# Performance work log

Hardware: AMD Instinct MI355X
Metric: run time of the kernel (lower is better)

Reference implementation:

```python
import jax, jax.numpy as jnp
import numpy as np

DEPTH = 3
MAX_NB = 10
HIDDEN = 128


def setup_inputs() -> dict:
    key = jax.random.key(0)
    k = jax.random.split(key, 14)
    B, A, E, H, NB = 64, 1024, 2048, HIDDEN, MAX_NB
    s = 0.05
    return {
        "input_atom": jax.random.normal(k[0], (B, A, 82), jnp.float32),
        "input_bond": jax.random.normal(k[1], (B, E, 6), jnp.float32),
        "atom_graph": jax.random.randint(k[2], (B, A, NB), 0, A),
        "bond_graph": jax.random.randint(k[3], (B, A, NB), 0, E),
        "num_nbs": jax.random.randint(k[4], (B, A), 0, NB + 1),
        "node_mask": jnp.ones((B, A), jnp.float32),
        "W_atom": jax.random.normal(k[5], (82, H), jnp.float32) * s,
        "W_nei_atom": jax.random.normal(k[6], (H, H), jnp.float32) * s,
        "W_nei_bond": jax.random.normal(k[7], (6, H), jnp.float32) * s,
        "W_self": jax.random.normal(k[8], (H, H), jnp.float32) * s,
        "W_U2": jax.random.normal(k[9], (H + 6, H), jnp.float32) * s,
        "b_U2": jax.random.normal(k[10], (H,), jnp.float32) * s,
        "W_U1": jax.random.normal(k[11], (2 * H, H), jnp.float32) * s,
        "b_U1": jax.random.normal(k[12], (H,), jnp.float32) * s,
    }


def reference(input_atom, input_bond, atom_graph, bond_graph, num_nbs, node_mask,
              W_atom, W_nei_atom, W_nei_bond, W_self, W_U2, b_U2, W_U1, b_U1):
    B, A, NB = atom_graph.shape
    H = W_atom.shape[1]
    atom_features = input_atom @ W_atom                       # [B, A, H]
    # neighbor validity mask: [B, A, NB, 1]
    mask_nei = (jnp.arange(NB)[None, None, :] < num_nbs[:, :, None]).astype(jnp.float32)[..., None]
    idx_a = atom_graph.reshape(B, A * NB, 1)
    idx_b = bond_graph.reshape(B, A * NB, 1)
    # bond neighbor features are loop-invariant: gather once
    fbond_nei = jnp.take_along_axis(input_bond, idx_b, axis=1).reshape(B, A, NB, 6)
    h_nei_bond = fbond_nei @ W_nei_bond                       # [B, A, NB, H]
    node_m = node_mask[..., None]                             # [B, A, 1]
    kernel = None
    for _ in range(DEPTH):
        fatom_nei = jnp.take_along_axis(atom_features, idx_a, axis=1).reshape(B, A, NB, H)
        h_nei = (fatom_nei @ W_nei_atom) * h_nei_bond         # [B, A, NB, H]
        f_nei = jnp.sum(h_nei * mask_nei, axis=2)             # [B, A, H]
        f_self = atom_features @ W_self                        # [B, A, H]
        kernel = f_nei * f_self * node_m
        l_nei = jnp.concatenate([fatom_nei, fbond_nei], axis=3)  # [B, A, NB, H+6]
        pre_label = l_nei @ W_U2 + b_U2
        nei_label = jnp.sum(pre_label * mask_nei, axis=2)      # [B, A, H]
        new_label = jnp.concatenate([atom_features, nei_label], axis=2)
        atom_features = new_label @ W_U1 + b_U1
    return kernel, atom_features
```

## Files before the change

### kernel.cpp

```cpp
#include <hip/hip_runtime.h>

constexpr int NB = 10, H = 128;
constexpr int M = 64 * 1024;
constexpr long SL = (long)M * H;

typedef __attribute__((ext_vector_type(8))) short s16x8;
typedef __attribute__((ext_vector_type(4))) float f32x4;

__device__ __forceinline__ ushort f2b(float f) {
    union { float f; uint u; } v; v.f = f;
    uint u = v.u;
    uint r = u + 0x7fffu + ((u >> 16) & 1u);
    return (ushort)(r >> 16);
}
__device__ __forceinline__ float b2f(ushort u) {
    union { uint u; float f; } v; v.u = ((uint)u) << 16; return v.f;
}

__device__ __forceinline__ int swz(int bid, int cpx) {
    return (bid & 7) * cpx + (bid >> 3);
}

template<int NC, int FLAGS>
__device__ __forceinline__ void gemm_body(
    int tg, const ushort* __restrict__ Abf, const ushort* __restrict__ WT,
    const ushort* __restrict__ FNb, const float* __restrict__ nmask,
    float* __restrict__ Cf, ushort* __restrict__ Cb)
{
    constexpr bool KOUT = FLAGS & 8, OF32 = FLAGS & 16;
    constexpr int K = NC * 32;
    const int lane = threadIdx.x & 63, wid = threadIdx.x >> 6;
    const int l15 = lane & 15, g = lane >> 4;

    s16x8 w[2][NC];
    #pragma unroll
    for (int ct = 0; ct < 2; ++ct)
        #pragma unroll
        for (int kc = 0; kc < NC; ++kc)
            w[ct][kc] = *(const s16x8*)(WT + (size_t)((2 * wid + ct) * 16 + l15) * K + kc * 32 + g * 8);

    #pragma unroll
    for (int i = 0; i < 4; ++i) {
        const int m0 = (tg * 4 + i) * 16;
        s16x8 ac[NC];
        #pragma unroll
        for (int kc = 0; kc < NC; ++kc)
            ac[kc] = *(const s16x8*)(Abf + (size_t)(m0 + l15) * K + kc * 32 + g * 8);

        f32x4 acc[2];
        #pragma unroll
        for (int ct = 0; ct < 2; ++ct) acc[ct] = (f32x4){0.f, 0.f, 0.f, 0.f};
        #pragma unroll
        for (int kc = 0; kc < NC; ++kc)
            #pragma unroll
            for (int ct = 0; ct < 2; ++ct)
                acc[ct] = __builtin_amdgcn_mfma_f32_16x16x32_bf16(ac[kc], w[ct][kc], acc[ct], 0, 0, 0);

        #pragma unroll
        for (int ct = 0; ct < 2; ++ct) {
            const int col = (2 * wid + ct) * 16 + l15;
            #pragma unroll
            for (int r = 0; r < 4; ++r) {
                const int m = m0 + 4 * g + r;
                const size_t o = (size_t)m * H + col;
                float v = acc[ct][r];
                if constexpr (KOUT) v = v * b2f(FNb[o]) * nmask[m];
                if constexpr (OF32) Cf[o] = v; else Cb[o] = f2b(v);
            }
        }
    }
}

template<bool OF32>
__device__ __forceinline__ void u1f_body(
    int tg, const ushort* __restrict__ AF, const ushort* __restrict__ SATOM,
    const ushort* __restrict__ FBSb, const ushort* __restrict__ WT,
    float* __restrict__ Cf, ushort* __restrict__ Cb)
{
    const int lane = threadIdx.x & 63, wid = threadIdx.x >> 6;
    const int l15 = lane & 15, g = lane >> 4;

    s16x8 w[2][9];
    #pragma unroll
    for (int ct = 0; ct < 2; ++ct)
        #pragma unroll
        for (int kc = 0; kc < 9; ++kc)
            w[ct][kc] = *(const s16x8*)(WT + (size_t)((2 * wid + ct) * 16 + l15) * 288 + kc * 32 + g * 8);
    #pragma unroll
    for (int ct = 0; ct < 2; ++ct)
        #pragma unroll
        for (int kc = 0; kc < 9; ++kc)
            asm volatile("" : "+v"(w[ct][kc]));

    #pragma unroll
    for (int i = 0; i < 4; ++i) {
        const int m0 = (tg * 4 + i) * 16;
        const size_t rb = (size_t)(m0 + l15) * H + g * 8;
        s16x8 ac[9];
        #pragma unroll
        for (int kc = 0; kc < 4; ++kc) {
            ac[kc]     = *(const s16x8*)(AF    + rb + kc * 32);
            ac[kc + 4] = *(const s16x8*)(SATOM + rb + kc * 32);
        }
        ac[8] = (s16x8){0,0,0,0,0,0,0,0};
        if (g == 0) ac[8] = *(const s16x8*)(FBSb + (size_t)(m0 + l15) * 8);

        f32x4 acc[2];
        #pragma unroll
        for (int ct = 0; ct < 2; ++ct) acc[ct] = (f32x4){0.f, 0.f, 0.f, 0.f};
        #pragma unroll
        for (int kc = 0; kc < 9; ++kc)
            #pragma unroll
            for (int ct = 0; ct < 2; ++ct)
                acc[ct] = __builtin_amdgcn_mfma_f32_16x16x32_bf16(ac[kc], w[ct][kc], acc[ct], 0, 0, 0);

        #pragma unroll
        for (int ct = 0; ct < 2; ++ct) {
            const int col = (2 * wid + ct) * 16 + l15;
            #pragma unroll
            for (int r = 0; r < 4; ++r) {
                const size_t o = (size_t)(m0 + 4 * g + r) * H + col;
                if constexpr (OF32) Cf[o] = acc[ct][r]; else Cb[o] = f2b(acc[ct][r]);
            }
        }
    }
}

template<int NC, int FLAGS>
__global__ __launch_bounds__(256, 4) void gemm_af(
    const ushort* __restrict__ Abf, const ushort* __restrict__ WT,
    const ushort* __restrict__ FNb, const float* __restrict__ nmask,
    float* __restrict__ Cf, ushort* __restrict__ Cb)
{
    gemm_body<NC, FLAGS>(swz(blockIdx.x, 128), Abf, WT, FNb, nmask, Cf, Cb);
}

template<bool OF32>
__global__ __launch_bounds__(256, 3) void u1f(
    const ushort* __restrict__ AF, const ushort* __restrict__ SATOM,
    const ushort* __restrict__ FBSb, const ushort* __restrict__ WT,
    float* __restrict__ Cf, ushort* __restrict__ Cb)
{
    u1f_body<OF32>(swz(blockIdx.x, 128), AF, SATOM, FBSb, WT, Cf, Cb);
}

__global__ __launch_bounds__(256, 3) void final2(
    const ushort* __restrict__ AF, const ushort* __restrict__ SATl,
    const ushort* __restrict__ FBSb, const ushort* __restrict__ WTu1f,
    const ushort* __restrict__ WTslf, const ushort* __restrict__ FNEIb,
    const float* __restrict__ nmask, float* __restrict__ out1,
    float* __restrict__ out0)
{
    if (blockIdx.x < 1024)
        u1f_body<true>(swz(blockIdx.x, 128), AF, SATl, FBSb, WTu1f, out1, nullptr);
    else
        gemm_body<4, 8 | 16>(swz(blockIdx.x - 1024, 128), AF, WTslf, FNEIb,
                             nmask, out0, nullptr);
}

__global__ __launch_bounds__(256, 8) void gather_satom(
    const ushort* __restrict__ AF, const int* __restrict__ ag,
    const int* __restrict__ nn, ushort* __restrict__ SATOM)
{
    const int bid = swz(blockIdx.x, 512);
    const int m  = bid * 16 + (threadIdx.x >> 4);
    const int c8 = (threadIdx.x & 15) * 8;
    const int b  = m >> 10;
    const int nnb = nn[m];
    const ushort* AFb = AF + ((size_t)b << 10) * H + c8;
    const int* agm = ag + (size_t)m * NB;

    int2 iv0 = *(const int2*)(agm + 0);
    int2 iv1 = *(const int2*)(agm + 2);
    int2 iv2 = *(const int2*)(agm + 4);
    int2 iv3 = *(const int2*)(agm + 6);
    int2 iv4 = *(const int2*)(agm + 8);

    float sacc[8];
    #pragma unroll
    for (int i = 0; i < 8; ++i) sacc[i] = 0.f;

    #define GS_STEP(nb, ia)                                              \
    if ((nb) < nnb) {                                                    \
        s16x8 av = *(const s16x8*)(AFb + (size_t)(ia) * H);              \
        _Pragma("unroll")                                                \
        for (int i = 0; i < 8; ++i) sacc[i] += b2f((ushort)av[i]);       \
    }
    GS_STEP(0, iv0.x) GS_STEP(1, iv0.y)
    GS_STEP(2, iv1.x) GS_STEP(3, iv1.y)
    GS_STEP(4, iv2.x) GS_STEP(5, iv2.y)
    GS_STEP(6, iv3.x) GS_STEP(7, iv3.y)
    GS_STEP(8, iv4.x) GS_STEP(9, iv4.y)
    #undef GS_STEP

    s16x8 so;
    #pragma unroll
    for (int i = 0; i < 8; ++i) so[i] = (short)f2b(sacc[i]);
    *(s16x8*)(SATOM + (size_t)m * H + c8) = so;
}

__global__ __launch_bounds__(256, 4) void gather_last(
    const ushort* __restrict__ AF, const ushort* __restrict__ ATW,
    const ushort* __restrict__ HB, const int* __restrict__ ag,
    const int* __restrict__ bg, const int* __restrict__ nn,
    ushort* __restrict__ SATOM, ushort* __restrict__ FNEIb)
{
    const int bid = swz(blockIdx.x, 512);
    const int m  = bid * 16 + (threadIdx.x >> 4);
    const int c8 = (threadIdx.x & 15) * 8;
    const int b  = m >> 10;
    const int nnb = nn[m];
    const ushort* AFb  = AF  + ((size_t)b << 10) * H + c8;
    const ushort* ATWb = ATW + ((size_t)b << 10) * H + c8;
    const ushort* HBb  = HB  + ((size_t)b << 11) * H + c8;
    const int* agm = ag + (size_t)m * NB;
    const int* bgm = bg + (size_t)m * NB;

    int2 ia0 = *(const int2*)(agm + 0), ib0 = *(const int2*)(bgm + 0);
    int2 ia1 = *(const int2*)(agm + 2), ib1 = *(const int2*)(bgm + 2);
    int2 ia2 = *(const int2*)(agm + 4), ib2 = *(const int2*)(bgm + 4);
    int2 ia3 = *(const int2*)(agm + 6), ib3 = *(const int2*)(bgm + 6);
    int2 ia4 = *(const int2*)(agm + 8), ib4 = *(const int2*)(bgm + 8);

    float sacc[8], facc[8];
    #pragma unroll
    for (int i = 0; i < 8; ++i) { sacc[i] = 0.f; facc[i] = 0.f; }

    #define GL_STEP(nb, ia, ib)                                          \
    if ((nb) < nnb) {                                                    \
        s16x8 av = *(const s16x8*)(AFb  + (size_t)(ia) * H);             \
        s16x8 tv = *(const s16x8*)(ATWb + (size_t)(ia) * H);             \
        s16x8 hv = *(const s16x8*)(HBb  + (size_t)(ib) * H);             \
        _Pragma("unroll")                                                \
        for (int i = 0; i < 8; ++i) {                                    \
            sacc[i] += b2f((ushort)av[i]);                               \
            facc[i] += b2f((ushort)tv[i]) * b2f((ushort)hv[i]);          \
        }                                                                \
    }
    GL_STEP(0, ia0.x, ib0.x) GL_STEP(1, ia0.y, ib0.y)
    GL_STEP(2, ia1.x, ib1.x) GL_STEP(3, ia1.y, ib1.y)
    GL_STEP(4, ia2.x, ib2.x) GL_STEP(5, ia2.y, ib2.y)
    GL_STEP(6, ia3.x, ib3.x) GL_STEP(7, ia3.y, ib3.y)
    GL_STEP(8, ia4.x, ib4.x) GL_STEP(9, ia4.y, ib4.y)
    #undef GL_STEP

    s16x8 so, fo;
    #pragma unroll
    for (int i = 0; i < 8; ++i) { so[i] = (short)f2b(sacc[i]); fo[i] = (short)f2b(facc[i]); }
    *(s16x8*)(SATOM + (size_t)m * H + c8) = so;
    *(s16x8*)(FNEIb + (size_t)m * H + c8) = fo;
}

__device__ __forceinline__ void fa_body(
    int tg, const float* __restrict__ ia, const float* __restrict__ Wa,
    ushort* __restrict__ Cb)
{
    const int lane = threadIdx.x & 63, wid = threadIdx.x >> 6;
    const int l15 = lane & 15, g = lane >> 4;

    s16x8 w[2][3];
    #pragma unroll
    for (int ct = 0; ct < 2; ++ct) {
        const int n = (2 * wid + ct) * 16 + l15;
        #pragma unroll
        for (int kc = 0; kc < 3; ++kc) {
            s16x8 wv;
            #pragma unroll
            for (int i = 0; i < 8; ++i) {
                const int k = kc * 32 + g * 8 + i;
                wv[i] = (short)(k < 82 ? f2b(Wa[k * H + n]) : 0);
            }
            w[ct][kc] = wv;
        }
    }

    #pragma unroll
    for (int t = 0; t < 4; ++t) {
        const int m0 = (tg * 4 + t) * 16;
        const float* row = ia + (size_t)(m0 + l15) * 82;
        s16x8 a[3];
        #pragma unroll
        for (int kc = 0; kc < 3; ++kc) {
            #pragma unroll
            for (int p = 0; p < 4; ++p) {
                const int k = kc * 32 + g * 8 + 2 * p;
                float2 v = (k < 82) ? *(const float2*)(row + k)
                                    : make_float2(0.f, 0.f);
                a[kc][2 * p]     = (short)f2b(v.x);
                a[kc][2 * p + 1] = (short)f2b(v.y);
            }
        }
        f32x4 acc[2];
        #pragma unroll
        for (int ct = 0; ct < 2; ++ct) acc[ct] = (f32x4){0.f, 0.f, 0.f, 0.f};
        #pragma unroll
        for (int kc = 0; kc < 3; ++kc)
            #pragma unroll
            for (int ct = 0; ct < 2; ++ct)
                acc[ct] = __builtin_amdgcn_mfma_f32_16x16x32_bf16(a[kc], w[ct][kc], acc[ct], 0, 0, 0);
        #pragma unroll
        for (int ct = 0; ct < 2; ++ct) {
            const int col = (2 * wid + ct) * 16 + l15;
            #pragma unroll
            for (int r = 0; r < 4; ++r)
                Cb[(size_t)(m0 + 4 * g + r) * H + col] = f2b(acc[ct][r]);
        }
    }
}

__global__ __launch_bounds__(256, 4) void k0_prep_fa(
    const float* __restrict__ ia, const float* __restrict__ Wa,
    const float* __restrict__ Wna, const float* __restrict__ Ws,
    const float* __restrict__ Wu2, const float* __restrict__ bu2,
    const float* __restrict__ Wu1, const float* __restrict__ bu1,
    const float* __restrict__ bond, const int* __restrict__ bg,
    const int* __restrict__ nn, const float* __restrict__ Wnb,
    ushort* __restrict__ AF0, ushort* __restrict__ WTs,
    ushort* __restrict__ FBSb, ushort* __restrict__ HB)
{
    const int bid = blockIdx.x;
    if (bid < 1024) {
        fa_body(swz(bid, 128), ia, Wa, AF0);
    } else if (bid < 1296) {
        int t = (bid - 1024) * 256 + threadIdx.x;
        const int tid = t;
        if (t < 128 * 128) { int n = t / 128, k = t % 128;
            WTs[tid] = f2b(Wna[k * H + n]); return; }
        t -= 128 * 128;
        if (t < 128 * 128) { int n = t / 128, k = t % 128;
            WTs[tid] = f2b(Ws[k * H + n]); return; }
        t -= 128 * 128;
        {
            const int n = t / 288, k = t % 288;
            float v = 0.f;
            if (k < 128) {
                v = Wu1[k * H + n];
            } else if (k < 256) {
                const int kk = k - 128;
                float s = 0.f;
                for (int j = 0; j < 128; ++j) s += Wu2[kk * H + j] * Wu1[(128 + j) * H + n];
                v = s;
            } else {
                const int j = k - 256;
                if (j < 6) {
                    float s = 0.f;
                    for (int q = 0; q < 128; ++q) s += Wu2[(128 + j) * H + q] * Wu1[(128 + q) * H + n];
                    v = s;
                } else if (j == 6) {
                    float s = 0.f;
                    for (int q = 0; q < 128; ++q) s += bu2[q] * Wu1[(128 + q) * H + n];
                    v = s;
                } else if (j == 7) {
                    v = bu1[n];
                }
            }
            WTs[tid] = f2b(v);
            return;
        }
    } else if (bid < 1552) {
        const int m = (bid - 1296) * 256 + threadIdx.x;
        const int b = m >> 10;
        const int nnb = nn[m];
        float s[6] = {0,0,0,0,0,0};
        for (int nb = 0; nb < nnb; ++nb) {
            const int ib = bg[m * NB + nb];
            const float* fb = bond + ((size_t)(b << 11) + (size_t)ib) * 6;
            #pragma unroll
            for (int j = 0; j < 6; ++j) s[j] += fb[j];
        }
        s16x8 o;
        #pragma unroll
        for (int j = 0; j < 6; ++j) o[j] = (short)f2b(s[j]);
        o[6] = (short)f2b((float)nnb);
        o[7] = (short)f2b(1.0f);
        *(s16x8*)(FBSb + (size_t)m * 8) = o;
    } else {
        const int t = (bid - 1552) * 256 + threadIdx.x;
        const int r = t >> 4, c8 = (t & 15) * 8;
        const float* fb = bond + (size_t)r * 6;
        const float2 f01 = *(const float2*)fb;
        const float2 f23 = *(const float2*)(fb + 2);
        const float2 f45 = *(const float2*)(fb + 4);
        s16x8 o;
        #pragma unroll
        for (int i = 0; i < 8; ++i) {
            const int c = c8 + i;
            const float v = f01.x * Wnb[0 * H + c] + f01.y * Wnb[1 * H + c]
                          + f23.x * Wnb[2 * H + c] + f23.y * Wnb[3 * H + c]
                          + f45.x * Wnb[4 * H + c] + f45.y * Wnb[5 * H + c];
            o[i] = (short)f2b(v);
        }
        *(s16x8*)(HB + (size_t)r * H + c8) = o;
    }
}

extern "C" void kernel_launch(void* const* d_in, const int* in_sizes, int n_in,
                              void* d_out, int out_size, void* d_ws, size_t ws_size,
                              hipStream_t stream)
{
    (void)in_sizes; (void)n_in; (void)out_size; (void)ws_size;

    const float* input_atom = (const float*)d_in[0];
    const float* input_bond = (const float*)d_in[1];
    const int*   atom_graph = (const int*)d_in[2];
    const int*   bond_graph = (const int*)d_in[3];
    const int*   num_nbs    = (const int*)d_in[4];
    const float* node_mask  = (const float*)d_in[5];
    const float* W_atom     = (const float*)d_in[6];
    const float* W_nei_atom = (const float*)d_in[7];
    const float* W_nei_bond = (const float*)d_in[8];
    const float* W_self     = (const float*)d_in[9];
    const float* W_U2       = (const float*)d_in[10];
    const float* b_U2       = (const float*)d_in[11];
    const float* W_U1       = (const float*)d_in[12];
    const float* b_U1       = (const float*)d_in[13];

    char* ws = (char*)d_ws;
    const size_t MB = 1024 * 1024;
    ushort* AF0   = (ushort*)(ws);
    ushort* AF1   = (ushort*)(ws + 16 * MB);
    ushort* SATw  = (ushort*)(ws + 32 * MB);
    ushort* ATW   = SATw;
    ushort* HB    = (ushort*)(ws + 64 * MB);
    ushort* SATl  = (ushort*)(ws + 96 * MB);
    ushort* FBSb  = (ushort*)(ws + 112 * MB);
    ushort* WTs_  = (ushort*)(ws + 113 * MB);

    ushort* WTna  = WTs_;
    ushort* WTslf = WTna  + 128 * 128;
    ushort* WTu1f = WTslf + 128 * 128;

    float*  out0  = (float*)d_out;
    float*  out1  = out0 + SL;
    ushort* FNEIb = AF1;

    k0_prep_fa<<<9744, 256, 0, stream>>>(input_atom, W_atom, W_nei_atom,
                                         W_self, W_U2, b_U2, W_U1, b_U1,
                                         input_bond, bond_graph, num_nbs,
                                         W_nei_bond, AF0, WTs_, FBSb, HB);

    gather_satom<<<4096, 256, 0, stream>>>(AF0, atom_graph, num_nbs, SATw);
    u1f<false><<<1024, 256, 0, stream>>>(AF0, SATw, FBSb, WTu1f, nullptr, AF1);
    gather_satom<<<4096, 256, 0, stream>>>(AF1, atom_graph, num_nbs, SATw);
    u1f<false><<<1024, 256, 0, stream>>>(AF1, SATw, FBSb, WTu1f, nullptr, AF0);

    gemm_af<4, 0><<<1024, 256, 0, stream>>>(AF0, WTna, nullptr, nullptr,
                                            nullptr, ATW);
    gather_last<<<4096, 256, 0, stream>>>(AF0, ATW, HB, atom_graph, bond_graph,
                                          num_nbs, SATl, FNEIb);
    final2<<<2048, 256, 0, stream>>>(AF0, SATl, FBSb, WTu1f, WTslf, FNEIb,
                                     node_mask, out1, out0);
}
```

Measured before the change: 185.5 us.

## Move self-projection GEMM earlier and fuse kernel output into last gather

The W_self projection now runs in the same launch as the W_nei_atom projection and writes a bf16 SLF buffer. The last gather kernel multiplies its neighbor sum by SLF and the node mask and writes the fp32 kernel output directly, so the bf16 FNEI intermediate and its reload are gone. The final launch is reduced to the plain U1 GEMM. This removes one 16 MB intermediate round trip, but the SLF read now sits in the gather kernel and the U1 launch is no longer paired with another GEMM.

```diff
diff --git a/kernel.cpp b/kernel.cpp
--- a/kernel.cpp
+++ b/kernel.cpp
@@ -21,13 +21,11 @@
     return (bid & 7) * cpx + (bid >> 3);
 }
 
-template<int NC, int FLAGS>
+template<int NC>
 __device__ __forceinline__ void gemm_body(
     int tg, const ushort* __restrict__ Abf, const ushort* __restrict__ WT,
-    const ushort* __restrict__ FNb, const float* __restrict__ nmask,
-    float* __restrict__ Cf, ushort* __restrict__ Cb)
-{
-    constexpr bool KOUT = FLAGS & 8, OF32 = FLAGS & 16;
+    ushort* __restrict__ Cb)
+{
     constexpr int K = NC * 32;
     const int lane = threadIdx.x & 63, wid = threadIdx.x >> 6;
     const int l15 = lane & 15, g = lane >> 4;
@@ -60,13 +58,8 @@
         for (int ct = 0; ct < 2; ++ct) {
             const int col = (2 * wid + ct) * 16 + l15;
             #pragma unroll
-            for (int r = 0; r < 4; ++r) {
-                const int m = m0 + 4 * g + r;
-                const size_t o = (size_t)m * H + col;
-                float v = acc[ct][r];
-                if constexpr (KOUT) v = v * b2f(FNb[o]) * nmask[m];
-                if constexpr (OF32) Cf[o] = v; else Cb[o] = f2b(v);
-            }
+            for (int r = 0; r < 4; ++r)
+                Cb[(size_t)(m0 + 4 * g + r) * H + col] = f2b(acc[ct][r]);
         }
     }
 }
@@ -126,15 +119,6 @@
     }
 }
 
-template<int NC, int FLAGS>
-__global__ __launch_bounds__(256, 4) void gemm_af(
-    const ushort* __restrict__ Abf, const ushort* __restrict__ WT,
-    const ushort* __restrict__ FNb, const float* __restrict__ nmask,
-    float* __restrict__ Cf, ushort* __restrict__ Cb)
-{
-    gemm_body<NC, FLAGS>(swz(blockIdx.x, 128), Abf, WT, FNb, nmask, Cf, Cb);
-}
-
 template<bool OF32>
 __global__ __launch_bounds__(256, 3) void u1f(
     const ushort* __restrict__ AF, const ushort* __restrict__ SATOM,
@@ -144,18 +128,15 @@
     u1f_body<OF32>(swz(blockIdx.x, 128), AF, SATOM, FBSb, WT, Cf, Cb);
 }
 
-__global__ __launch_bounds__(256, 3) void final2(
-    const ushort* __restrict__ AF, const ushort* __restrict__ SATl,
-    const ushort* __restrict__ FBSb, const ushort* __restrict__ WTu1f,
-    const ushort* __restrict__ WTslf, const ushort* __restrict__ FNEIb,
-    const float* __restrict__ nmask, float* __restrict__ out1,
-    float* __restrict__ out0)
+__global__ __launch_bounds__(256, 4) void k5_atw_slf(
+    const ushort* __restrict__ AF, const ushort* __restrict__ WTna,
+    const ushort* __restrict__ WTslf, ushort* __restrict__ ATW,
+    ushort* __restrict__ SLF)
 {
     if (blockIdx.x < 1024)
-        u1f_body<true>(swz(blockIdx.x, 128), AF, SATl, FBSb, WTu1f, out1, nullptr);
+        gemm_body<4>(swz(blockIdx.x, 128), AF, WTna, ATW);
     else
-        gemm_body<4, 8 | 16>(swz(blockIdx.x - 1024, 128), AF, WTslf, FNEIb,
-                             nmask, out0, nullptr);
+        gemm_body<4>(swz(blockIdx.x - 1024, 128), AF, WTslf, SLF);
 }
 
 __global__ __launch_bounds__(256, 8) void gather_satom(
@@ -199,11 +180,12 @@
     *(s16x8*)(SATOM + (size_t)m * H + c8) = so;
 }
 
-__global__ __launch_bounds__(256, 4) void gather_last(
+__global__ __launch_bounds__(256, 4) void gather_last2(
     const ushort* __restrict__ AF, const ushort* __restrict__ ATW,
-    const ushort* __restrict__ HB, const int* __restrict__ ag,
+    const ushort* __restrict__ HB, const ushort* __restrict__ SLF,
+    const float* __restrict__ nmask, const int* __restrict__ ag,
     const int* __restrict__ bg, const int* __restrict__ nn,
-    ushort* __restrict__ SATOM, ushort* __restrict__ FNEIb)
+    ushort* __restrict__ SATOM, float* __restrict__ out0)
 {
     const int bid = swz(blockIdx.x, 512);
     const int m  = bid * 16 + (threadIdx.x >> 4);
@@ -244,11 +226,21 @@
     GL_STEP(8, ia4.x, ib4.x) GL_STEP(9, ia4.y, ib4.y)
     #undef GL_STEP
 
-    s16x8 so, fo;
-    #pragma unroll
-    for (int i = 0; i < 8; ++i) { so[i] = (short)f2b(sacc[i]); fo[i] = (short)f2b(facc[i]); }
+    s16x8 so;
+    #pragma unroll
+    for (int i = 0; i < 8; ++i) so[i] = (short)f2b(sacc[i]);
     *(s16x8*)(SATOM + (size_t)m * H + c8) = so;
-    *(s16x8*)(FNEIb + (size_t)m * H + c8) = fo;
+
+    const float nm = nmask[m];
+    s16x8 sv = *(const s16x8*)(SLF + (size_t)m * H + c8);
+    f32x4 lo, hi;
+    #pragma unroll
+    for (int i = 0; i < 4; ++i) {
+        lo[i] = facc[i]     * b2f((ushort)sv[i])     * nm;
+        hi[i] = facc[i + 4] * b2f((ushort)sv[i + 4]) * nm;
+    }
+    *(f32x4*)(out0 + (size_t)m * H + c8)     = lo;
+    *(f32x4*)(out0 + (size_t)m * H + c8 + 4) = hi;
 }
 
 __device__ __forceinline__ void fa_body(
@@ -432,7 +424,7 @@
 
     float*  out0  = (float*)d_out;
     float*  out1  = out0 + SL;
-    ushort* FNEIb = AF1;
+    ushort* SLF   = AF1;
 
     k0_prep_fa<<<9744, 256, 0, stream>>>(input_atom, W_atom, W_nei_atom,
                                          W_self, W_U2, b_U2, W_U1, b_U1,
@@ -444,10 +436,9 @@
     gather_satom<<<4096, 256, 0, stream>>>(AF1, atom_graph, num_nbs, SATw);
     u1f<false><<<1024, 256, 0, stream>>>(AF1, SATw, FBSb, WTu1f, nullptr, AF0);
 
-    gemm_af<4, 0><<<1024, 256, 0, stream>>>(AF0, WTna, nullptr, nullptr,
-                                            nullptr, ATW);
-    gather_last<<<4096, 256, 0, stream>>>(AF0, ATW, HB, atom_graph, bond_graph,
-                                          num_nbs, SATl, FNEIb);
-    final2<<<2048, 256, 0, stream>>>(AF0, SATl, FBSb, WTu1f, WTslf, FNEIb,
-                                     node_mask, out1, out0);
-}
+    k5_atw_slf<<<2048, 256, 0, stream>>>(AF0, WTna, WTslf, ATW, SLF);
+    gather_last2<<<4096, 256, 0, stream>>>(AF0, ATW, HB, SLF, node_mask,
+                                           atom_graph, bond_graph, num_nbs,
+                                           SATl, out0);
+    u1f<true><<<1024, 256, 0, stream>>>(AF0, SATl, FBSb, WTu1f, out1, nullptr);
+}
```

Result: no change. 186.2 us (+0.4%).
